# Kernel tuning notes

Hardware: AMD Instinct MI355X
Metric: run time of the kernel (lower is better)

Reference implementation:

```python
import jax, jax.numpy as jnp
import numpy as np

NUM_HEADS = 16

def _apply_rope(t, cos, sin):
    # t: [B, nh, S, hd]; cos/sin: [S, hd//2]
    t1 = t[..., 0::2]
    t2 = t[..., 1::2]
    c = cos[None, None, :, :]
    s = sin[None, None, :, :]
    r1 = t1 * c - t2 * s
    r2 = t1 * s + t2 * c
    # interleave back to [..., hd]
    out = jnp.stack([r1, r2], axis=-1)
    return out.reshape(t.shape)

def setup_inputs() -> dict:
    key = jax.random.key(0)
    ks = jax.random.split(key, 6)
    B, S, H = 1, 4096, 1024
    hd = H // NUM_HEADS
    x = jax.random.normal(ks[0], (B, S, H), dtype=jnp.float32)
    # RoPE angle matrix: theta[pos, i] = pos / 10000^(2i/hd), shape [context, hd//2]
    pos = jnp.arange(S, dtype=jnp.float32)[:, None]
    inv_freq = 1.0 / (10000.0 ** (jnp.arange(0, hd, 2, dtype=jnp.float32) / hd))
    rotation = pos * inv_freq[None, :]
    sc = 1.0 / np.sqrt(H)
    W_qkv = jax.random.normal(ks[1], (H, 3 * H), dtype=jnp.float32) * sc
    b_qkv = jax.random.normal(ks[2], (3 * H,), dtype=jnp.float32) * 0.01
    W_out = jax.random.normal(ks[3], (H, H), dtype=jnp.float32) * sc
    b_out = jax.random.normal(ks[4], (H,), dtype=jnp.float32) * 0.01
    return {"x": x, "rotation": rotation, "W_qkv": W_qkv, "b_qkv": b_qkv,
            "W_out": W_out, "b_out": b_out, "window_size": 33}

def reference(x, rotation, W_qkv, b_qkv, W_out, b_out, window_size):
    B, S, H = x.shape
    nh = NUM_HEADS
    hd = H // nh
    W = window_size
    pad = W // 2
    qkv = x @ W_qkv + b_qkv                               # [B, S, 3H]
    qkv = qkv.reshape(B, S, nh, 3 * hd).transpose(0, 2, 1, 3)  # [B, nh, S, 3hd]
    q, k, v = jnp.split(qkv, 3, axis=-1)                  # each [B, nh, S, hd]
    cos = jnp.cos(rotation[:S])
    sin = jnp.sin(rotation[:S])
    q = _apply_rope(q, cos, sin)
    k = _apply_rope(k, cos, sin)
    # zero-pad along sequence, then gather sliding windows
    k_pad = jnp.pad(k, ((0, 0), (0, 0), (pad, pad), (0, 0)))
    v_pad = jnp.pad(v, ((0, 0), (0, 0), (pad, pad), (0, 0)))
    idx = jnp.arange(S)[:, None] + jnp.arange(W)[None, :]  # [S, W]
    k_win = k_pad[:, :, idx, :]                            # [B, nh, S, W, hd]
    v_win = v_pad[:, :, idx, :]
    scores = jnp.einsum('bnsh,bnswh->bnsw', q, k_win) / np.sqrt(hd)
    attn = jax.nn.softmax(scores, axis=-1)
    ctx = jnp.einsum('bnsw,bnswh->bnsh', attn, v_win)      # [B, nh, S, hd]
    ctx = ctx.transpose(0, 2, 1, 3).reshape(B, S, H)
    return ctx @ W_out + b_out
```

## Files before the change

### kernel.cpp

```cpp
#include <hip/hip_runtime.h>
#include <hip/hip_bf16.h>

#define S_LEN 4096
#define NH 16
#define HD 64
#define WIN 33
#define PAD 16
#define QT 64
#define KROWS 96
#define KPITCH_U 36

#define BM 128
#define BN 128
#define BK 64

typedef short short8 __attribute__((ext_vector_type(8)));
typedef float f32x4 __attribute__((ext_vector_type(4)));

__device__ __forceinline__ float bl(unsigned u){ return __uint_as_float(u << 16); }
__device__ __forceinline__ float bh(unsigned u){ return __uint_as_float(u & 0xffff0000u); }
__device__ __forceinline__ unsigned f2bfu(float f){
  unsigned u = __float_as_uint(f);
  return (u + 0x7fffu + ((u >> 16) & 1u)) >> 16;
}
__device__ __forceinline__ unsigned pack2(float a, float b){ return f2bfu(a) | (f2bfu(b) << 16); }

__device__ __forceinline__ void gload_lds16(const void* g, void* l){
  __builtin_amdgcn_global_load_lds(
      (const __attribute__((address_space(1))) void*)g,
      (__attribute__((address_space(3))) void*)l, 16, 0, 0);
}


__global__ __launch_bounds__(256) void prep_all(
    const float* __restrict__ rot, float2* __restrict__ csq,
    const float* __restrict__ x, __hip_bfloat16* __restrict__ xb,
    const float* __restrict__ Wq, __hip_bfloat16* __restrict__ Wt1,
    const float* __restrict__ Wo, __hip_bfloat16* __restrict__ Wt2)
{
  __shared__ float tile[32][33];
  const int b = blockIdx.x, tid = threadIdx.x;
  if (b < 512) {
    int t = b * 256 + tid;
    float v = rot[t], sv, cv;
    __sincosf(v, &sv, &cv);
    csq[t] = make_float2(cv, sv);
  } else if (b < 2560) {
    int t = (b - 512) * 256 + tid;
    const float4* p = (const float4*)x + (size_t)t * 2;
    float4 a = p[0], c = p[1];
    uint4 o;
    o.x = pack2(a.x, a.y); o.y = pack2(a.z, a.w);
    o.z = pack2(c.x, c.y); o.w = pack2(c.z, c.w);
    ((uint4*)xb)[t] = o;
  } else {
    const float* in; unsigned short* out; int R, C, bx, by;
    if (b < 5632) { int bb = b - 2560; in = Wq; out = (unsigned short*)Wt1; R = 1024; C = 3072; bx = bb % 96; by = bb / 96; }
    else          { int bb = b - 5632; in = Wo; out = (unsigned short*)Wt2; R = 1024; C = 1024; bx = bb % 32; by = bb / 32; }
    int c0 = bx * 32, r0 = by * 32;
    int tx = tid & 31, ty = tid >> 5;
    #pragma unroll
    for (int i = 0; i < 4; ++i) {
      int r = ty + i * 8;
      tile[r][tx] = in[(size_t)(r0 + r) * C + c0 + tx];
    }
    __syncthreads();
    #pragma unroll
    for (int i = 0; i < 4; ++i) {
      int cc = ty + i * 8;
      out[(size_t)(c0 + cc) * R + r0 + tx] = (unsigned short)f2bfu(tile[tx][cc]);
    }
  }
}


__global__ __launch_bounds__(256) void gemm_qkv_rope(
    const __hip_bfloat16* __restrict__ A,
    const __hip_bfloat16* __restrict__ Bt,
    const float* __restrict__ bias,
    const float2* __restrict__ csq,
    unsigned short* __restrict__ Cout,
    int M, int N, int K)
{
  __shared__ unsigned int lA[2][BM * BK / 2];
  __shared__ unsigned int lB[2][BN * BK / 2];
  const int tid = threadIdx.x;
  const int wave = tid >> 6, lane = tid & 63;
  const int flat = blockIdx.y * 24 + blockIdx.x;
  const int xcd = flat & 7, local = flat >> 3;
  const int m0 = (local & 31) * BM;
  const int n0 = (xcd * 3 + (local >> 5)) * BN;
  const int wm = (wave >> 1) * 64, wn = (wave & 1) * 64;
  const int l16 = lane >> 4, l15 = lane & 15;

  f32x4 acc[4][4];
  #pragma unroll
  for (int i = 0; i < 4; ++i)
    #pragma unroll
    for (int j = 0; j < 4; ++j) acc[i][j] = (f32x4){0.f, 0.f, 0.f, 0.f};

  auto stage = [&](int buf, int kt) {
    #pragma unroll
    for (int it = 0; it < 4; ++it) {
      const int c = it * 256 + wave * 64 + lane;
      const int r = c >> 3, s8 = c & 7;
      const int ss = s8 ^ (r & 7);
      gload_lds16(A  + (size_t)(m0 + r) * K + kt * BK + ss * 8,
                  (char*)lA[buf] + (it * 256 + wave * 64) * 16);
      gload_lds16(Bt + (size_t)(n0 + r) * K + kt * BK + ss * 8,
                  (char*)lB[buf] + (it * 256 + wave * 64) * 16);
    }
  };

  const int nkt = K / BK;
  stage(0, 0);
  int cur = 0;
  for (int kt = 0; kt < nkt; ++kt) {
    const bool pf = (kt + 1 < nkt);
    if (pf) stage(cur ^ 1, kt + 1);
    if (pf) asm volatile("s_waitcnt vmcnt(8)" ::: "memory");
    else    asm volatile("s_waitcnt vmcnt(0)" ::: "memory");
    __builtin_amdgcn_s_barrier();
    __builtin_amdgcn_sched_barrier(0);
    #pragma unroll
    for (int ks = 0; ks < 2; ++ks) {
      short8 af[4], bfr[4];
      #pragma unroll
      for (int mi = 0; mi < 4; ++mi) {
        const int r = wm + mi * 16 + l15;
        const int slot = (ks * 4 + l16) ^ (r & 7);
        uint4 u = *(const uint4*)((const char*)lA[cur] + r * 128 + slot * 16);
        af[mi] = __builtin_bit_cast(short8, u);
      }
      #pragma unroll
      for (int ni = 0; ni < 4; ++ni) {
        const int r = wn + ni * 16 + l15;
        const int slot = (ks * 4 + l16) ^ (r & 7);
        uint4 u = *(const uint4*)((const char*)lB[cur] + r * 128 + slot * 16);
        bfr[ni] = __builtin_bit_cast(short8, u);
      }
      __builtin_amdgcn_s_setprio(1);
      #pragma unroll
      for (int mi = 0; mi < 4; ++mi)
        #pragma unroll
        for (int ni = 0; ni < 4; ++ni)
          acc[mi][ni] = __builtin_amdgcn_mfma_f32_16x16x32_bf16(af[mi], bfr[ni], acc[mi][ni], 0, 0, 0);
      __builtin_amdgcn_s_setprio(0);
    }
    __builtin_amdgcn_sched_barrier(0);
    __builtin_amdgcn_s_barrier();
    cur ^= 1;
  }

  #pragma unroll
  for (int ni = 0; ni < 4; ++ni) {
    const int cn = n0 + wn + ni * 16 + l15;
    const int rseg = cn % 192;
    const float bv = bias[cn];
    if (rseg < 128) {
      const int i = (rseg & 63) >> 1;
      const float sgn = (cn & 1) ? 1.f : -1.f;
      #pragma unroll
      for (int mi = 0; mi < 4; ++mi) {
        #pragma unroll
        for (int j = 0; j < 4; ++j) {
          const int rm = m0 + wm + mi * 16 + l16 * 4 + j;
          const float v = acc[mi][ni][j] + bv;
          const float p = __shfl_xor(v, 1);
          const float2 cs = csq[rm * 32 + i];
          Cout[(size_t)rm * N + cn] = (unsigned short)f2bfu(v * cs.x + p * (sgn * cs.y));
        }
      }
    } else {
      #pragma unroll
      for (int mi = 0; mi < 4; ++mi) {
        #pragma unroll
        for (int j = 0; j < 4; ++j) {
          const int rm = m0 + wm + mi * 16 + l16 * 4 + j;
          Cout[(size_t)rm * N + cn] = (unsigned short)f2bfu(acc[mi][ni][j] + bv);
        }
      }
    }
  }
}


__global__ __launch_bounds__(256) void gemm_out(
    const __hip_bfloat16* __restrict__ A,
    const __hip_bfloat16* __restrict__ Bt,
    const float* __restrict__ bias,
    float* __restrict__ Cout,
    int M, int N, int K)
{
  __shared__ unsigned int lA[2][128 * 64 / 2];
  __shared__ unsigned int lB[2][64 * 64 / 2];
  const int tid = threadIdx.x;
  const int wave = tid >> 6, lane = tid & 63;
  const int flat = blockIdx.y * 16 + blockIdx.x;
  const int xcd = flat & 7, local = flat >> 3;
  const int m0 = (local & 31) * 128;
  const int n0 = (xcd * 2 + (local >> 5)) * 64;
  const int wm = (wave >> 1) * 64, wn = (wave & 1) * 32;
  const int l16 = lane >> 4, l15 = lane & 15;

  f32x4 acc[4][2];
  #pragma unroll
  for (int i = 0; i < 4; ++i)
    #pragma unroll
    for (int j = 0; j < 2; ++j) acc[i][j] = (f32x4){0.f, 0.f, 0.f, 0.f};

  auto stage = [&](int buf, int kt) {
    #pragma unroll
    for (int it = 0; it < 4; ++it) {
      const int c = it * 256 + wave * 64 + lane;
      const int r = c >> 3, s8 = c & 7;
      const int ss = s8 ^ (r & 7);
      gload_lds16(A + (size_t)(m0 + r) * K + kt * 64 + ss * 8,
                  (char*)lA[buf] + (it * 256 + wave * 64) * 16);
    }
    #pragma unroll
    for (int it = 0; it < 2; ++it) {
      const int c = it * 256 + wave * 64 + lane;
      const int r = c >> 3, s8 = c & 7;
      const int ss = s8 ^ (r & 7);
      gload_lds16(Bt + (size_t)(n0 + r) * K + kt * 64 + ss * 8,
                  (char*)lB[buf] + (it * 256 + wave * 64) * 16);
    }
  };

  const int nkt = K / 64;
  stage(0, 0);
  int cur = 0;
  for (int kt = 0; kt < nkt; ++kt) {
    const bool pf = (kt + 1 < nkt);
    if (pf) stage(cur ^ 1, kt + 1);
    if (pf) asm volatile("s_waitcnt vmcnt(6)" ::: "memory");
    else    asm volatile("s_waitcnt vmcnt(0)" ::: "memory");
    __builtin_amdgcn_s_barrier();
    __builtin_amdgcn_sched_barrier(0);
    #pragma unroll
    for (int ks = 0; ks < 2; ++ks) {
      short8 af[4], bfr[2];
      #pragma unroll
      for (int mi = 0; mi < 4; ++mi) {
        const int r = wm + mi * 16 + l15;
        const int slot = (ks * 4 + l16) ^ (r & 7);
        uint4 u = *(const uint4*)((const char*)lA[cur] + r * 128 + slot * 16);
        af[mi] = __builtin_bit_cast(short8, u);
      }
      #pragma unroll
      for (int ni = 0; ni < 2; ++ni) {
        const int r = wn + ni * 16 + l15;
        const int slot = (ks * 4 + l16) ^ (r & 7);
        uint4 u = *(const uint4*)((const char*)lB[cur] + r * 128 + slot * 16);
        bfr[ni] = __builtin_bit_cast(short8, u);
      }
      __builtin_amdgcn_s_setprio(1);
      #pragma unroll
      for (int mi = 0; mi < 4; ++mi)
        #pragma unroll
        for (int ni = 0; ni < 2; ++ni)
          acc[mi][ni] = __builtin_amdgcn_mfma_f32_16x16x32_bf16(af[mi], bfr[ni], acc[mi][ni], 0, 0, 0);
      __builtin_amdgcn_s_setprio(0);
    }
    __builtin_amdgcn_sched_barrier(0);
    __builtin_amdgcn_s_barrier();
    cur ^= 1;
  }

  #pragma unroll
  for (int ni = 0; ni < 2; ++ni) {
    const int cn = n0 + wn + ni * 16 + l15;
    const float bv = bias[cn];
    #pragma unroll
    for (int mi = 0; mi < 4; ++mi) {
      #pragma unroll
      for (int j = 0; j < 4; ++j) {
        const int rm = m0 + wm + mi * 16 + l16 * 4 + j;
        Cout[(size_t)rm * N + cn] = acc[mi][ni][j] + bv;
      }
    }
  }
}


__global__ __launch_bounds__(256) void attn_kernel(const __hip_bfloat16* __restrict__ qkv,
                                                   __hip_bfloat16* __restrict__ ctx){
  __shared__ unsigned int kbuf[KROWS * KPITCH_U];
  __shared__ unsigned int vbuf[KROWS * KPITCH_U];
  const int tid = threadIdx.x;
  const int h   = blockIdx.x & 15;
  const int qs0 = (blockIdx.x >> 4) * QT;

  #pragma unroll
  for (int it = 0; it < 3; ++it) {
    int c = tid + it * 256;
    int r = c >> 3, s8 = c & 7;
    int srow = qs0 - PAD + r;
    uint4 kv = make_uint4(0, 0, 0, 0), vv = make_uint4(0, 0, 0, 0);
    if ((unsigned)srow < (unsigned)S_LEN) {
      kv = ((const uint4*)(qkv + (size_t)srow * 3072 + h * 192 + 64))[s8];
      vv = ((const uint4*)(qkv + (size_t)srow * 3072 + h * 192 + 128))[s8];
    }
    *(uint4*)(kbuf + r * KPITCH_U + s8 * 4) = kv;
    *(uint4*)(vbuf + r * KPITCH_U + s8 * 4) = vv;
  }

  const int ql = tid >> 2, t4 = tid & 3;
  const uint4* qp = (const uint4*)(qkv + (size_t)(qs0 + ql) * 3072 + h * 192);
  float qf[64];
  #pragma unroll
  for (int c = 0; c < 8; ++c) {
    uint4 v = qp[c];
    qf[c*8+0] = bl(v.x); qf[c*8+1] = bh(v.x);
    qf[c*8+2] = bl(v.y); qf[c*8+3] = bh(v.y);
    qf[c*8+4] = bl(v.z); qf[c*8+5] = bh(v.z);
    qf[c*8+6] = bl(v.w); qf[c*8+7] = bh(v.w);
  }
  __syncthreads();

  float sc[9];
  #pragma unroll
  for (int j = 0; j < 9; ++j) sc[j] = 0.f;
  float mx = -1e30f;
  #pragma unroll
  for (int j = 0; j < 9; ++j) {
    int w = t4 + 4 * j;
    if (w < WIN) {
      int rw = ql + w;
      const uint4* kp = (const uint4*)(kbuf + rw * KPITCH_U);
      float d = 0.f;
      #pragma unroll
      for (int c = 0; c < 8; ++c) {
        uint4 kv = kp[c];
        d += qf[c*8+0]*bl(kv.x) + qf[c*8+1]*bh(kv.x)
           + qf[c*8+2]*bl(kv.y) + qf[c*8+3]*bh(kv.y)
           + qf[c*8+4]*bl(kv.z) + qf[c*8+5]*bh(kv.z)
           + qf[c*8+6]*bl(kv.w) + qf[c*8+7]*bh(kv.w);
      }
      sc[j] = d * 0.125f;
      mx = fmaxf(mx, sc[j]);
    }
  }
  mx = fmaxf(mx, __shfl_xor(mx, 1));
  mx = fmaxf(mx, __shfl_xor(mx, 2));
  float sum = 0.f;
  #pragma unroll
  for (int j = 0; j < 9; ++j) {
    int w = t4 + 4 * j;
    if (w < WIN) { sc[j] = __expf(sc[j] - mx); sum += sc[j]; }
  }
  sum += __shfl_xor(sum, 1);
  sum += __shfl_xor(sum, 2);
  const float inv = 1.0f / sum;
  #pragma unroll
  for (int j = 0; j < 9; ++j) sc[j] *= inv;

  float accd[16];
  #pragma unroll
  for (int i = 0; i < 16; ++i) accd[i] = 0.f;
  #pragma unroll
  for (int w = 0; w < WIN; ++w) {
    float wgt = __shfl(sc[w >> 2], ((tid & 63) & ~3) | (w & 3), 64);
    int rw = ql + w;
    const uint4* vp = (const uint4*)(vbuf + rw * KPITCH_U + t4 * 8);
    uint4 a = vp[0], b = vp[1];
    float vf[16];
    vf[0]=bl(a.x); vf[1]=bh(a.x); vf[2]=bl(a.y); vf[3]=bh(a.y);
    vf[4]=bl(a.z); vf[5]=bh(a.z); vf[6]=bl(a.w); vf[7]=bh(a.w);
    vf[8]=bl(b.x); vf[9]=bh(b.x); vf[10]=bl(b.y); vf[11]=bh(b.y);
    vf[12]=bl(b.z); vf[13]=bh(b.z); vf[14]=bl(b.w); vf[15]=bh(b.w);
    #pragma unroll
    for (int i = 0; i < 16; ++i) accd[i] += wgt * vf[i];
  }

  unsigned short* op = (unsigned short*)ctx + (size_t)(qs0 + ql) * 1024 + h * 64 + t4 * 16;
  uint4 o1, o2;
  o1.x = pack2(accd[0], accd[1]);  o1.y = pack2(accd[2], accd[3]);
  o1.z = pack2(accd[4], accd[5]);  o1.w = pack2(accd[6], accd[7]);
  o2.x = pack2(accd[8], accd[9]);  o2.y = pack2(accd[10], accd[11]);
  o2.z = pack2(accd[12], accd[13]); o2.w = pack2(accd[14], accd[15]);
  *(uint4*)op = o1;
  *((uint4*)op + 1) = o2;
}


extern "C" void kernel_launch(void* const* d_in, const int* in_sizes, int n_in,
                              void* d_out, int out_size, void* d_ws, size_t ws_size,
                              hipStream_t stream)
{
  const float* x     = (const float*)d_in[0];
  const float* rot   = (const float*)d_in[1];
  const float* W_qkv = (const float*)d_in[2];
  const float* b_qkv = (const float*)d_in[3];
  const float* W_out = (const float*)d_in[4];
  const float* b_out = (const float*)d_in[5];
  float* out = (float*)d_out;

  char* ws = (char*)d_ws;
  __hip_bfloat16* xb   = (__hip_bfloat16*)(ws + 0);
  __hip_bfloat16* Wt1  = (__hip_bfloat16*)(ws + 8388608);
  __hip_bfloat16* Wt2  = (__hip_bfloat16*)(ws + 14680064);
  __hip_bfloat16* qkvb = (__hip_bfloat16*)(ws + 16777216);
  __hip_bfloat16* ctx  = (__hip_bfloat16*)(ws + 41943040);
  float2* csq          = (float2*)(ws + 50331648);

  prep_all<<<6656, 256, 0, stream>>>(rot, csq, x, xb, W_qkv, Wt1, W_out, Wt2);
  gemm_qkv_rope<<<dim3(3072 / BN, 4096 / BM), 256, 0, stream>>>(xb, Wt1, b_qkv, csq,
                                                                (unsigned short*)qkvb, 4096, 3072, 1024);
  attn_kernel<<<64 * 16, 256, 0, stream>>>(qkvb, ctx);
  gemm_out<<<dim3(1024 / 64, 4096 / 128), 256, 0, stream>>>(ctx, Wt2, b_out, out, 4096, 1024, 1024);
}
```

Measured before the change: 96.98 us.

## Enlarge QKV GEMM tiles to 256x256 with 8 waves and drop XCD swizzle

The QKV+RoPE GEMM moves from 128x128 tiles with 4 waves to 256x256 tiles with 8 waves. Each wave now owns a 128x64 sub-tile, and the inner loop is reordered to load A fragments once per half and stream B fragments. LDS per block doubles to 128 KB. The grid shrinks to 192 blocks, which is under one wave of CUs on MI355X. The XCD-aware block remapping is removed from both GEMMs in favour of plain blockIdx mapping. The aim is more operand reuse per LDS byte, at the cost of lower occupancy, a partial CU fill, and more register pressure from 32 accumulator tiles.

```diff
diff --git a/kernel.cpp b/kernel.cpp
--- a/kernel.cpp
+++ b/kernel.cpp
@@ -9,10 +9,6 @@
 #define QT 64
 #define KROWS 96
 #define KPITCH_U 36
-
-#define BM 128
-#define BN 128
-#define BK 64
 
 typedef short short8 __attribute__((ext_vector_type(8)));
 typedef float f32x4 __attribute__((ext_vector_type(4)));
@@ -74,7 +70,7 @@
 }
 
 
-__global__ __launch_bounds__(256) void gemm_qkv_rope(
+__global__ __launch_bounds__(512, 2) void gemm_qkv_rope(
     const __hip_bfloat16* __restrict__ A,
     const __hip_bfloat16* __restrict__ Bt,
     const float* __restrict__ bias,
@@ -82,37 +78,34 @@
     unsigned short* __restrict__ Cout,
     int M, int N, int K)
 {
-  __shared__ unsigned int lA[2][BM * BK / 2];
-  __shared__ unsigned int lB[2][BN * BK / 2];
+  __shared__ unsigned int lA[2][256 * 64 / 2];
+  __shared__ unsigned int lB[2][256 * 64 / 2];
   const int tid = threadIdx.x;
   const int wave = tid >> 6, lane = tid & 63;
-  const int flat = blockIdx.y * 24 + blockIdx.x;
-  const int xcd = flat & 7, local = flat >> 3;
-  const int m0 = (local & 31) * BM;
-  const int n0 = (xcd * 3 + (local >> 5)) * BN;
-  const int wm = (wave >> 1) * 64, wn = (wave & 1) * 64;
+  const int m0 = blockIdx.y * 256, n0 = blockIdx.x * 256;
+  const int wm = (wave >> 2) * 128, wn = (wave & 3) * 64;
   const int l16 = lane >> 4, l15 = lane & 15;
 
-  f32x4 acc[4][4];
-  #pragma unroll
-  for (int i = 0; i < 4; ++i)
+  f32x4 acc[8][4];
+  #pragma unroll
+  for (int i = 0; i < 8; ++i)
     #pragma unroll
     for (int j = 0; j < 4; ++j) acc[i][j] = (f32x4){0.f, 0.f, 0.f, 0.f};
 
   auto stage = [&](int buf, int kt) {
     #pragma unroll
     for (int it = 0; it < 4; ++it) {
-      const int c = it * 256 + wave * 64 + lane;
+      const int c = it * 512 + tid;
       const int r = c >> 3, s8 = c & 7;
       const int ss = s8 ^ (r & 7);
-      gload_lds16(A  + (size_t)(m0 + r) * K + kt * BK + ss * 8,
-                  (char*)lA[buf] + (it * 256 + wave * 64) * 16);
-      gload_lds16(Bt + (size_t)(n0 + r) * K + kt * BK + ss * 8,
-                  (char*)lB[buf] + (it * 256 + wave * 64) * 16);
+      gload_lds16(A  + (size_t)(m0 + r) * K + kt * 64 + ss * 8,
+                  (char*)lA[buf] + c * 16);
+      gload_lds16(Bt + (size_t)(n0 + r) * K + kt * 64 + ss * 8,
+                  (char*)lB[buf] + c * 16);
     }
   };
 
-  const int nkt = K / BK;
+  const int nkt = K / 64;
   stage(0, 0);
   int cur = 0;
   for (int kt = 0; kt < nkt; ++kt) {
@@ -123,29 +116,41 @@
     __builtin_amdgcn_s_barrier();
     __builtin_amdgcn_sched_barrier(0);
     #pragma unroll
-    for (int ks = 0; ks < 2; ++ks) {
-      short8 af[4], bfr[4];
-      #pragma unroll
-      for (int mi = 0; mi < 4; ++mi) {
-        const int r = wm + mi * 16 + l15;
-        const int slot = (ks * 4 + l16) ^ (r & 7);
-        uint4 u = *(const uint4*)((const char*)lA[cur] + r * 128 + slot * 16);
-        af[mi] = __builtin_bit_cast(short8, u);
-      }
-      #pragma unroll
-      for (int ni = 0; ni < 4; ++ni) {
-        const int r = wn + ni * 16 + l15;
-        const int slot = (ks * 4 + l16) ^ (r & 7);
-        uint4 u = *(const uint4*)((const char*)lB[cur] + r * 128 + slot * 16);
-        bfr[ni] = __builtin_bit_cast(short8, u);
-      }
-      __builtin_amdgcn_s_setprio(1);
+    for (int mh = 0; mh < 2; ++mh) {
+      short8 af[4][2];
       #pragma unroll
       for (int mi = 0; mi < 4; ++mi)
         #pragma unroll
-        for (int ni = 0; ni < 4; ++ni)
-          acc[mi][ni] = __builtin_amdgcn_mfma_f32_16x16x32_bf16(af[mi], bfr[ni], acc[mi][ni], 0, 0, 0);
-      __builtin_amdgcn_s_setprio(0);
+        for (int ks = 0; ks < 2; ++ks) {
+          const int r = wm + mh * 64 + mi * 16 + l15;
+          const int slot = (ks * 4 + l16) ^ (r & 7);
+          uint4 u = *(const uint4*)((const char*)lA[cur] + r * 128 + slot * 16);
+          af[mi][ks] = __builtin_bit_cast(short8, u);
+        }
+      #pragma unroll
+      for (int nh = 0; nh < 2; ++nh) {
+        short8 bfr[2][2];
+        #pragma unroll
+        for (int ni = 0; ni < 2; ++ni)
+          #pragma unroll
+          for (int ks = 0; ks < 2; ++ks) {
+            const int r = wn + nh * 32 + ni * 16 + l15;
+            const int slot = (ks * 4 + l16) ^ (r & 7);
+            uint4 u = *(const uint4*)((const char*)lB[cur] + r * 128 + slot * 16);
+            bfr[ni][ks] = __builtin_bit_cast(short8, u);
+          }
+        __builtin_amdgcn_s_setprio(1);
+        #pragma unroll
+        for (int ks = 0; ks < 2; ++ks)
+          #pragma unroll
+          for (int mi = 0; mi < 4; ++mi)
+            #pragma unroll
+            for (int ni = 0; ni < 2; ++ni)
+              acc[mh * 4 + mi][nh * 2 + ni] =
+                  __builtin_amdgcn_mfma_f32_16x16x32_bf16(af[mi][ks], bfr[ni][ks],
+                                                          acc[mh * 4 + mi][nh * 2 + ni], 0, 0, 0);
+        __builtin_amdgcn_s_setprio(0);
+      }
     }
     __builtin_amdgcn_sched_barrier(0);
     __builtin_amdgcn_s_barrier();
@@ -161,7 +166,7 @@
       const int i = (rseg & 63) >> 1;
       const float sgn = (cn & 1) ? 1.f : -1.f;
       #pragma unroll
-      for (int mi = 0; mi < 4; ++mi) {
+      for (int mi = 0; mi < 8; ++mi) {
         #pragma unroll
         for (int j = 0; j < 4; ++j) {
           const int rm = m0 + wm + mi * 16 + l16 * 4 + j;
@@ -173,7 +178,7 @@
       }
     } else {
       #pragma unroll
-      for (int mi = 0; mi < 4; ++mi) {
+      for (int mi = 0; mi < 8; ++mi) {
         #pragma unroll
         for (int j = 0; j < 4; ++j) {
           const int rm = m0 + wm + mi * 16 + l16 * 4 + j;
@@ -196,10 +201,7 @@
   __shared__ unsigned int lB[2][64 * 64 / 2];
   const int tid = threadIdx.x;
   const int wave = tid >> 6, lane = tid & 63;
-  const int flat = blockIdx.y * 16 + blockIdx.x;
-  const int xcd = flat & 7, local = flat >> 3;
-  const int m0 = (local & 31) * 128;
-  const int n0 = (xcd * 2 + (local >> 5)) * 64;
+  const int m0 = blockIdx.y * 128, n0 = blockIdx.x * 64;
   const int wm = (wave >> 1) * 64, wn = (wave & 1) * 32;
   const int l16 = lane >> 4, l15 = lane & 15;
 
@@ -406,8 +408,8 @@
   float2* csq          = (float2*)(ws + 50331648);
 
   prep_all<<<6656, 256, 0, stream>>>(rot, csq, x, xb, W_qkv, Wt1, W_out, Wt2);
-  gemm_qkv_rope<<<dim3(3072 / BN, 4096 / BM), 256, 0, stream>>>(xb, Wt1, b_qkv, csq,
-                                                                (unsigned short*)qkvb, 4096, 3072, 1024);
+  gemm_qkv_rope<<<dim3(3072 / 256, 4096 / 256), 512, 0, stream>>>(xb, Wt1, b_qkv, csq,
+                                                                  (unsigned short*)qkvb, 4096, 3072, 1024);
   attn_kernel<<<64 * 16, 256, 0, stream>>>(qkvb, ctx);
   gemm_out<<<dim3(1024 / 64, 4096 / 128), 256, 0, stream>>>(ctx, Wt2, b_out, out, 4096, 1024, 1024);
 }
```

Result: no change. 95.53 us (-1.5%).

## Shrink QKV GEMM tile to 128x96, single-buffer LDS, drop XCD swizzle

Applied to the files above, without the earlier changes.

The QKV+RoPE GEMM tile changes from 128x128 to 128x96, giving 1024 blocks instead of 768. The double-buffered LDS prefetch pipeline is replaced by a single-buffered load/sync/compute loop, and a min-occupancy launch bound is added so more blocks fit per CU. The XCD-aware block swizzle is also removed from both GEMMs in favour of plain blockIdx mapping. The aim is better CU occupancy and a more even wave count, at the cost of losing load/compute overlap and L2 locality across XCDs.

```diff
diff --git a/kernel.cpp b/kernel.cpp
--- a/kernel.cpp
+++ b/kernel.cpp
@@ -9,10 +9,6 @@
 #define QT 64
 #define KROWS 96
 #define KPITCH_U 36
-
-#define BM 128
-#define BN 128
-#define BK 64
 
 typedef short short8 __attribute__((ext_vector_type(8)));
 typedef float f32x4 __attribute__((ext_vector_type(4)));
@@ -74,7 +70,7 @@
 }
 
 
-__global__ __launch_bounds__(256) void gemm_qkv_rope(
+__global__ __launch_bounds__(256, 4) void gemm_qkv_rope(
     const __hip_bfloat16* __restrict__ A,
     const __hip_bfloat16* __restrict__ Bt,
     const float* __restrict__ bias,
@@ -82,78 +78,65 @@
     unsigned short* __restrict__ Cout,
     int M, int N, int K)
 {
-  __shared__ unsigned int lA[2][BM * BK / 2];
-  __shared__ unsigned int lB[2][BN * BK / 2];
+  __shared__ unsigned int lA[128 * 64 / 2];
+  __shared__ unsigned int lB[96 * 64 / 2];
   const int tid = threadIdx.x;
   const int wave = tid >> 6, lane = tid & 63;
-  const int flat = blockIdx.y * 24 + blockIdx.x;
-  const int xcd = flat & 7, local = flat >> 3;
-  const int m0 = (local & 31) * BM;
-  const int n0 = (xcd * 3 + (local >> 5)) * BN;
-  const int wm = (wave >> 1) * 64, wn = (wave & 1) * 64;
+  const int m0 = blockIdx.y * 128, n0 = blockIdx.x * 96;
+  const int wm = (wave >> 1) * 64, wn = (wave & 1) * 48;
   const int l16 = lane >> 4, l15 = lane & 15;
 
-  f32x4 acc[4][4];
+  f32x4 acc[4][3];
   #pragma unroll
   for (int i = 0; i < 4; ++i)
     #pragma unroll
-    for (int j = 0; j < 4; ++j) acc[i][j] = (f32x4){0.f, 0.f, 0.f, 0.f};
-
-  auto stage = [&](int buf, int kt) {
+    for (int j = 0; j < 3; ++j) acc[i][j] = (f32x4){0.f, 0.f, 0.f, 0.f};
+
+  const int nkt = K / 64;
+  for (int kt = 0; kt < nkt; ++kt) {
+    __syncthreads();
     #pragma unroll
     for (int it = 0; it < 4; ++it) {
-      const int c = it * 256 + wave * 64 + lane;
+      const int c = it * 256 + tid;
       const int r = c >> 3, s8 = c & 7;
       const int ss = s8 ^ (r & 7);
-      gload_lds16(A  + (size_t)(m0 + r) * K + kt * BK + ss * 8,
-                  (char*)lA[buf] + (it * 256 + wave * 64) * 16);
-      gload_lds16(Bt + (size_t)(n0 + r) * K + kt * BK + ss * 8,
-                  (char*)lB[buf] + (it * 256 + wave * 64) * 16);
-    }
-  };
-
-  const int nkt = K / BK;
-  stage(0, 0);
-  int cur = 0;
-  for (int kt = 0; kt < nkt; ++kt) {
-    const bool pf = (kt + 1 < nkt);
-    if (pf) stage(cur ^ 1, kt + 1);
-    if (pf) asm volatile("s_waitcnt vmcnt(8)" ::: "memory");
-    else    asm volatile("s_waitcnt vmcnt(0)" ::: "memory");
-    __builtin_amdgcn_s_barrier();
-    __builtin_amdgcn_sched_barrier(0);
+      gload_lds16(A + (size_t)(m0 + r) * K + kt * 64 + ss * 8, (char*)lA + c * 16);
+    }
+    #pragma unroll
+    for (int it = 0; it < 3; ++it) {
+      const int c = it * 256 + tid;
+      const int r = c >> 3, s8 = c & 7;
+      const int ss = s8 ^ (r & 7);
+      gload_lds16(Bt + (size_t)(n0 + r) * K + kt * 64 + ss * 8, (char*)lB + c * 16);
+    }
+    __syncthreads();
     #pragma unroll
     for (int ks = 0; ks < 2; ++ks) {
-      short8 af[4], bfr[4];
+      short8 af[4], bfr[3];
       #pragma unroll
       for (int mi = 0; mi < 4; ++mi) {
         const int r = wm + mi * 16 + l15;
         const int slot = (ks * 4 + l16) ^ (r & 7);
-        uint4 u = *(const uint4*)((const char*)lA[cur] + r * 128 + slot * 16);
+        uint4 u = *(const uint4*)((const char*)lA + r * 128 + slot * 16);
         af[mi] = __builtin_bit_cast(short8, u);
       }
       #pragma unroll
-      for (int ni = 0; ni < 4; ++ni) {
+      for (int ni = 0; ni < 3; ++ni) {
         const int r = wn + ni * 16 + l15;
         const int slot = (ks * 4 + l16) ^ (r & 7);
-        uint4 u = *(const uint4*)((const char*)lB[cur] + r * 128 + slot * 16);
+        uint4 u = *(const uint4*)((const char*)lB + r * 128 + slot * 16);
         bfr[ni] = __builtin_bit_cast(short8, u);
       }
-      __builtin_amdgcn_s_setprio(1);
       #pragma unroll
       for (int mi = 0; mi < 4; ++mi)
         #pragma unroll
-        for (int ni = 0; ni < 4; ++ni)
+        for (int ni = 0; ni < 3; ++ni)
           acc[mi][ni] = __builtin_amdgcn_mfma_f32_16x16x32_bf16(af[mi], bfr[ni], acc[mi][ni], 0, 0, 0);
-      __builtin_amdgcn_s_setprio(0);
-    }
-    __builtin_amdgcn_sched_barrier(0);
-    __builtin_amdgcn_s_barrier();
-    cur ^= 1;
-  }
-
-  #pragma unroll
-  for (int ni = 0; ni < 4; ++ni) {
+    }
+  }
+
+  #pragma unroll
+  for (int ni = 0; ni < 3; ++ni) {
     const int cn = n0 + wn + ni * 16 + l15;
     const int rseg = cn % 192;
     const float bv = bias[cn];
@@ -196,10 +179,7 @@
   __shared__ unsigned int lB[2][64 * 64 / 2];
   const int tid = threadIdx.x;
   const int wave = tid >> 6, lane = tid & 63;
-  const int flat = blockIdx.y * 16 + blockIdx.x;
-  const int xcd = flat & 7, local = flat >> 3;
-  const int m0 = (local & 31) * 128;
-  const int n0 = (xcd * 2 + (local >> 5)) * 64;
+  const int m0 = blockIdx.y * 128, n0 = blockIdx.x * 64;
   const int wm = (wave >> 1) * 64, wn = (wave & 1) * 32;
   const int l16 = lane >> 4, l15 = lane & 15;
 
@@ -406,8 +386,8 @@
   float2* csq          = (float2*)(ws + 50331648);
 
   prep_all<<<6656, 256, 0, stream>>>(rot, csq, x, xb, W_qkv, Wt1, W_out, Wt2);
-  gemm_qkv_rope<<<dim3(3072 / BN, 4096 / BM), 256, 0, stream>>>(xb, Wt1, b_qkv, csq,
-                                                                (unsigned short*)qkvb, 4096, 3072, 1024);
+  gemm_qkv_rope<<<dim3(3072 / 96, 4096 / 128), 256, 0, stream>>>(xb, Wt1, b_qkv, csq,
+                                                                 (unsigned short*)qkvb, 4096, 3072, 1024);
   attn_kernel<<<64 * 16, 256, 0, stream>>>(qkvb, ctx);
   gemm_out<<<dim3(1024 / 64, 4096 / 128), 256, 0, stream>>>(ctx, Wt2, b_out, out, 4096, 1024, 1024);
 }
```

New measurement: 87.95 us. 1.1x faster.
